# Kernel tuning notes

Hardware: AMD Instinct MI355X
Metric: run time of the kernel (lower is better)

## Reference

```python
import jax, jax.numpy as jnp
import numpy as np

N = 8192       # batch_size
D = 128        # embedding dim
C = 1000       # num classes
EPS = 1e-8     # torch CosineSimilarity eps


def setup_inputs() -> dict:
    key = jax.random.key(0)
    k1, k2, k3, k4 = jax.random.split(key, 4)
    inst_embed = jax.random.normal(k1, (N, D), dtype=jnp.float32)
    proxy = jax.random.normal(k2, (N, D), dtype=jnp.float32)
    # binary mask marking same-class (non-negative) pairs, stored as float
    negative_mask = (jax.random.uniform(k3, (N, C)) < 0.5).astype(jnp.float32)
    labels = jax.random.randint(k4, (N,), 0, C)
    temperature = jnp.float32(0.07)
    margin = jnp.float32(0.0)
    return {
        'inst_embed': inst_embed,
        'proxy': proxy,
        'negative_mask': negative_mask,
        'labels': labels,
        'temperature': temperature,
        'margin': margin,
    }


def _remove_diag(M):
    # M: [h, h] -> [h, h-1], dropping the diagonal, row-major order (as torch bool-mask view)
    h = M.shape[0]
    j = jnp.arange(h - 1)[None, :]
    i = jnp.arange(h)[:, None]
    cols = j + (j >= i)  # skip column i in row i
    return jnp.take_along_axis(M, cols, axis=1)


def _l2_normalize(x):
    return x / jnp.maximum(jnp.linalg.norm(x, axis=-1, keepdims=True), EPS)


def reference(inst_embed, proxy, negative_mask, labels, temperature, margin):
    negative_mask = negative_mask.T                       # [C, N]
    xn = _l2_normalize(inst_embed)                        # [N, D]
    sim = xn @ xn.T                                       # [N, N] cosine similarity matrix
    instance_zone = jnp.exp((_remove_diag(sim) - margin) / temperature)  # [N, N-1]
    pn = _l2_normalize(proxy)
    inst2proxy_positive = jnp.exp((jnp.sum(xn * pn, axis=-1) - margin) / temperature)  # [N]
    # pos_collected_numerator == True branch
    mask_4_remove_negatives = _remove_diag(negative_mask[labels])        # [N, N-1]
    inst2inst_positives = instance_zone * mask_4_remove_negatives
    numerator = inst2proxy_positive + inst2inst_positives.sum(axis=1)
    denominator = inst2proxy_positive + instance_zone.sum(axis=1)
    criterion = -jnp.log(temperature * (numerator / denominator)).mean()
    return criterion
```

## Files before the change

### kernel.cpp

```cpp
#include <hip/hip_runtime.h>
#include <hip/hip_bf16.h>

typedef unsigned short u16;
typedef unsigned int   u32;
typedef unsigned long long u64;
typedef __attribute__((ext_vector_type(8))) short short8;
typedef __attribute__((ext_vector_type(4))) float float4v;

#define N 8192
#define D 128
#define C 1000
#define TILE 128
#define NW64 (N / 64)
#define JQ 4
#define GRIDY 16
#define JW (JQ * 2)
#define LOG2E 1.44269504088896340736f

__global__ void prep_kernel(const float* __restrict__ nm, u64* __restrict__ packed,
                            const float* __restrict__ x, const float* __restrict__ pr,
                            u16* __restrict__ xnb, float* __restrict__ p_out,
                            float* __restrict__ den, float* __restrict__ num,
                            const float* __restrict__ tp, const float* __restrict__ mp) {
    __shared__ u32 Ls[64 * 65];
    const int bid  = blockIdx.x;
    const int lane = threadIdx.x & 63;
    const int wv   = threadIdx.x >> 6;

    if (bid < 2048) {
        const int jt = bid & 127;
        const int lt = bid >> 7;
        const int j0 = jt * 64;
        const int l  = lt * 64 + lane;
        const bool lv = l < C;

        #pragma unroll
        for (int rr = 0; rr < 16; rr++) {
            const int r = wv * 16 + rr;
            float v = lv ? nm[(size_t)(j0 + r) * C + l] : 0.0f;
            Ls[r * 65 + lane] = (v > 0.5f) ? 1u : 0u;
        }
        __syncthreads();
        #pragma unroll
        for (int cc = 0; cc < 16; cc++) {
            const int c = wv * 16 + cc;
            u64 m = __ballot(Ls[lane * 65 + c] != 0u);
            if (lane == 0 && (lt * 64 + c) < C)
                packed[(size_t)(lt * 64 + c) * NW64 + jt] = m;
        }
    } else {
        const int row = (bid - 2048) * 4 + wv;
        const float2* xr  = (const float2*)(x  + (size_t)row * D);
        const float2* prr = (const float2*)(pr + (size_t)row * D);
        float2 xv = xr[lane];
        float2 pv = prr[lane];

        float sx  = xv.x * xv.x + xv.y * xv.y;
        float sp  = pv.x * pv.x + pv.y * pv.y;
        float sxp = xv.x * pv.x + xv.y * pv.y;
        #pragma unroll
        for (int off = 32; off; off >>= 1) {
            sx  += __shfl_xor(sx,  off);
            sp  += __shfl_xor(sp,  off);
            sxp += __shfl_xor(sxp, off);
        }
        float nx = fmaxf(sqrtf(sx), 1e-8f);
        float np = fmaxf(sqrtf(sp), 1e-8f);
        float inv = 1.0f / nx;

        __hip_bfloat16 b0 = __float2bfloat16(xv.x * inv);
        __hip_bfloat16 b1 = __float2bfloat16(xv.y * inv);
        ((__hip_bfloat162*)xnb)[(size_t)row * 64 + lane] = __halves2bfloat162(b0, b1);

        if (lane == 0) {
            float T = tp[0], M = mp[0];
            p_out[row] = __expf((sxp / (nx * np) - M) / T);
            den[row] = 0.0f;
            num[row] = 0.0f;
        }
    }
}

#define AS1 __attribute__((address_space(1)))
#define AS3 __attribute__((address_space(3)))

static __device__ __forceinline__ void load_lds16(const u16* g, u16* l) {
    __builtin_amdgcn_global_load_lds((const AS1 u32*)(const void*)g,
                                     (AS3 u32*)(void*)l, 16, 0, 0);
}

template <bool RELOAD>
__device__ __forceinline__ void mfma_chunk(float4v (&acc)[2][2], const short8 (&a_f)[4][2],
                                           short8 (&bc)[4][2], const u16* Bnext,
                                           const int (&koff)[4]) {
    #pragma unroll
    for (int a = 0; a < 2; a++)
        #pragma unroll
        for (int b = 0; b < 2; b++)
            acc[a][b] = (float4v){0.f, 0.f, 0.f, 0.f};
    #pragma unroll
    for (int kk = 0; kk < 4; kk++) {
        #pragma unroll
        for (int tm = 0; tm < 2; tm++)
            #pragma unroll
            for (int tn = 0; tn < 2; tn++)
                acc[tm][tn] = __builtin_amdgcn_mfma_f32_16x16x32_bf16(
                    a_f[kk][tm], bc[kk][tn], acc[tm][tn], 0, 0, 0);
        if (RELOAD) {
            #pragma unroll
            for (int tn = 0; tn < 2; tn++)
                bc[kk][tn] = *(const short8*)(Bnext + tn * 2048 + koff[kk]);
        }
    }
}

template <bool DIAG, int CI>
__device__ __forceinline__ void epi_chunk(const float4v (&acc)[2][2], const u64* __restrict__ Ms,
                                          float (&dacc)[2][4], float (&nacc)[2][4],
                                          int wv, int kq, int m0,
                                          int ibase, int jbase, int q,
                                          float kA2, float kB2) {
    #pragma unroll
    for (int tm = 0; tm < 2; tm++) {
        #pragma unroll
        for (int r = 0; r < 4; r++) {
            const int lrow = wv * 32 + tm * 16 + kq * 4 + r;
            const u64 ws = Ms[lrow * JW + q * 2 + (CI >> 1)] >> m0;
            const int gi = ibase + lrow;
            #pragma unroll
            for (int tn = 0; tn < 2; tn++) {
                float e = __builtin_amdgcn_exp2f(fmaf(acc[tm][tn][r], kA2, kB2));
                if (DIAG) {
                    const int gj = jbase + CI * 32 + tn * 16 + m0;
                    if (gi == gj) e = 0.0f;
                }
                dacc[tm][r] += e;
                const u32 bit = (u32)(ws >> (((CI & 1) * 2 + tn) * 16)) & 1u;
                nacc[tm][r] = fmaf((float)bit, e, nacc[tm][r]);
            }
        }
    }
}

__global__ __launch_bounds__(256, 2)
void cc_main(const u16* __restrict__ xnb, const int* __restrict__ labels,
             const u64* __restrict__ packed,
             float* __restrict__ den, float* __restrict__ num,
             const float* __restrict__ tp, const float* __restrict__ mp) {
    __shared__ u16 Bs[TILE * D];
    __shared__ u64 Ms[TILE * JW];

    const int tid  = threadIdx.x;
    const int lane = tid & 63;
    const int wv   = tid >> 6;
    const int m0   = lane & 15;
    const int kq   = lane >> 4;
    const int ibase  = blockIdx.x * TILE;
    const int jsplit = blockIdx.y;
    const int jt0    = jsplit * JQ;

    const float T = tp[0];
    const float M = mp[0];
    const float kA2 = LOG2E / T;
    const float kB2 = -M * LOG2E / T;

    #pragma unroll
    for (int t = 0; t < 4; t++) {
        const int idx = t * 256 + tid;
        const int row = idx >> 3, h = idx & 7;
        const int lab = labels[ibase + row];
        Ms[idx] = packed[(size_t)lab * NW64 + jt0 * 2 + h];
    }

    const u16* Alane = xnb + (size_t)(ibase + wv * 32 + m0) * D + kq * 8;
    short8 a_f[4][2];
    #pragma unroll
    for (int kk = 0; kk < 4; kk++)
        #pragma unroll
        for (int tm = 0; tm < 2; tm++)
            a_f[kk][tm] = *(const short8*)(Alane + tm * (16 * D) + kk * 32);

    const int srow  = wv * 4 + (lane >> 4);
    const int sunit = (lane & 15) ^ (srow & 7);
    const u16* Bsrc = xnb + (size_t)srow * D + sunit * 8;
    u16* BsDst = (u16*)Bs + wv * 512;

    const int swz7 = m0 & 7;
    int koff[4];
    #pragma unroll
    for (int kk = 0; kk < 4; kk++) koff[kk] = ((kq + kk * 4) ^ swz7) * 8;
    const u16* LBrd = (const u16*)Bs + m0 * 128;

    float dacc[2][4] = {};
    float nacc[2][4] = {};
    float4v acc[2][2];
    short8 bc[4][2];

    for (int q = 0; q < JQ; q++) {
        const int jt = jt0 + q;
        const int jbase = jt * TILE;
        const bool diag = (jt == blockIdx.x);

        __syncthreads();
        {
            const u16* sq = Bsrc + (size_t)jbase * D;
            #pragma unroll
            for (int rnd = 0; rnd < 8; rnd++)
                load_lds16(sq + rnd * 16 * D, BsDst + rnd * 2048);
        }
        __syncthreads();

        #pragma unroll
        for (int kk = 0; kk < 4; kk++)
            #pragma unroll
            for (int tn = 0; tn < 2; tn++)
                bc[kk][tn] = *(const short8*)(LBrd + tn * 2048 + koff[kk]);

        mfma_chunk<true>(acc, a_f, bc, LBrd + 1 * 4096, koff);
        if (diag) epi_chunk<true , 0>(acc, Ms, dacc, nacc, wv, kq, m0, ibase, jbase, q, kA2, kB2);
        else      epi_chunk<false, 0>(acc, Ms, dacc, nacc, wv, kq, m0, ibase, jbase, q, kA2, kB2);

        mfma_chunk<true>(acc, a_f, bc, LBrd + 2 * 4096, koff);
        if (diag) epi_chunk<true , 1>(acc, Ms, dacc, nacc, wv, kq, m0, ibase, jbase, q, kA2, kB2);
        else      epi_chunk<false, 1>(acc, Ms, dacc, nacc, wv, kq, m0, ibase, jbase, q, kA2, kB2);

        mfma_chunk<true>(acc, a_f, bc, LBrd + 3 * 4096, koff);
        if (diag) epi_chunk<true , 2>(acc, Ms, dacc, nacc, wv, kq, m0, ibase, jbase, q, kA2, kB2);
        else      epi_chunk<false, 2>(acc, Ms, dacc, nacc, wv, kq, m0, ibase, jbase, q, kA2, kB2);

        mfma_chunk<false>(acc, a_f, bc, LBrd, koff);
        if (diag) epi_chunk<true , 3>(acc, Ms, dacc, nacc, wv, kq, m0, ibase, jbase, q, kA2, kB2);
        else      epi_chunk<false, 3>(acc, Ms, dacc, nacc, wv, kq, m0, ibase, jbase, q, kA2, kB2);
    }

    #pragma unroll
    for (int tm = 0; tm < 2; tm++) {
        #pragma unroll
        for (int r = 0; r < 4; r++) {
            float d = dacc[tm][r], n = nacc[tm][r];
            #pragma unroll
            for (int off = 1; off < 16; off <<= 1) {
                d += __shfl_xor(d, off);
                n += __shfl_xor(n, off);
            }
            if (m0 == 0) {
                const int gi = ibase + wv * 32 + tm * 16 + kq * 4 + r;
                atomicAdd(&den[gi], d);
                atomicAdd(&num[gi], n);
            }
        }
    }
}

__global__ void loss_kernel(const float* __restrict__ p, const float* __restrict__ den,
                            const float* __restrict__ num, float* __restrict__ out,
                            const float* __restrict__ tp) {
    __shared__ float red[16];
    const float T = tp[0];
    float s = 0.0f;
    #pragma unroll
    for (int t = 0; t < N / 1024; t++) {
        const int i = t * 1024 + threadIdx.x;
        float pi = p[i];
        s += -__logf(T * (pi + num[i]) / (pi + den[i]));
    }
    #pragma unroll
    for (int off = 32; off; off >>= 1) s += __shfl_xor(s, off);
    const int lane = threadIdx.x & 63, wv = threadIdx.x >> 6;
    if (lane == 0) red[wv] = s;
    __syncthreads();
    if (wv == 0) {
        float t = (lane < 16) ? red[lane] : 0.0f;
        #pragma unroll
        for (int off = 8; off; off >>= 1) t += __shfl_xor(t, off);
        if (lane == 0) out[0] = t / (float)N;
    }
}

extern "C" void kernel_launch(void* const* d_in, const int* in_sizes, int n_in,
                              void* d_out, int out_size, void* d_ws, size_t ws_size,
                              hipStream_t stream) {
    (void)in_sizes; (void)n_in; (void)out_size; (void)ws_size;
    const float* inst   = (const float*)d_in[0];
    const float* proxy  = (const float*)d_in[1];
    const float* nm     = (const float*)d_in[2];
    const int*   labels = (const int*)d_in[3];
    const float* temp   = (const float*)d_in[4];
    const float* marg   = (const float*)d_in[5];
    float* out = (float*)d_out;

    char* ws = (char*)d_ws;
    u16*   xnb    = (u16*)ws;
    float* p_arr  = (float*)(ws + 2097152);
    u64*   packed = (u64*)(ws + 2129920);
    float* den    = (float*)(ws + 3153920);
    float* num    = (float*)(ws + 3186688);

    prep_kernel<<<4096, 256, 0, stream>>>(nm, packed, inst, proxy, xnb, p_arr,
                                          den, num, temp, marg);
    cc_main<<<dim3(N / TILE, GRIDY), 256, 0, stream>>>(xnb, labels, packed, den, num, temp, marg);
    loss_kernel<<<1, 1024, 0, stream>>>(p_arr, den, num, out, temp);
}
```

Before: 126.5 us.

## Double-buffer B tiles, vectorize mask packing, fuse loss into main kernel

The main GEMM loop now splits each 128-row B tile into two 64-row halves held in separate LDS buffers, so the next half loads while the current half is computed, replacing the load-then-compute pattern. The mask-packing stage reads the negative mask with float4 loads for full column blocks. The separate loss kernel is removed: the last block to finish, found through an atomic counter, computes the final reduction. This saves a launch and hides load latency, but the single finishing block runs the whole 8192-element reduction with only 256 threads.

```diff
diff --git a/kernel.cpp b/kernel.cpp
--- a/kernel.cpp
+++ b/kernel.cpp
@@ -14,6 +14,7 @@
 #define NW64 (N / 64)
 #define JQ 4
 #define GRIDY 16
+#define NBLK ((N / TILE) * GRIDY)
 #define JW (JQ * 2)
 #define LOG2E 1.44269504088896340736f
 
@@ -21,6 +22,7 @@
                             const float* __restrict__ x, const float* __restrict__ pr,
                             u16* __restrict__ xnb, float* __restrict__ p_out,
                             float* __restrict__ den, float* __restrict__ num,
+                            int* __restrict__ ctr,
                             const float* __restrict__ tp, const float* __restrict__ mp) {
     __shared__ u32 Ls[64 * 65];
     const int bid  = blockIdx.x;
@@ -31,14 +33,29 @@
         const int jt = bid & 127;
         const int lt = bid >> 7;
         const int j0 = jt * 64;
-        const int l  = lt * 64 + lane;
-        const bool lv = l < C;
-
-        #pragma unroll
-        for (int rr = 0; rr < 16; rr++) {
-            const int r = wv * 16 + rr;
-            float v = lv ? nm[(size_t)(j0 + r) * C + l] : 0.0f;
-            Ls[r * 65 + lane] = (v > 0.5f) ? 1u : 0u;
+        const int l0 = lt * 64;
+
+        if (lt < 15) {
+            const int tid = threadIdx.x;
+            #pragma unroll
+            for (int it = 0; it < 4; it++) {
+                const int r  = it * 16 + (tid >> 4);
+                const int c0 = (tid & 15) * 4;
+                const float4 v = *(const float4*)(nm + (size_t)(j0 + r) * C + l0 + c0);
+                Ls[r * 65 + c0 + 0] = (v.x > 0.5f) ? 1u : 0u;
+                Ls[r * 65 + c0 + 1] = (v.y > 0.5f) ? 1u : 0u;
+                Ls[r * 65 + c0 + 2] = (v.z > 0.5f) ? 1u : 0u;
+                Ls[r * 65 + c0 + 3] = (v.w > 0.5f) ? 1u : 0u;
+            }
+        } else {
+            const int l  = l0 + lane;
+            const bool lv = l < C;
+            #pragma unroll
+            for (int rr = 0; rr < 16; rr++) {
+                const int r = wv * 16 + rr;
+                float v = lv ? nm[(size_t)(j0 + r) * C + l] : 0.0f;
+                Ls[r * 65 + lane] = (v > 0.5f) ? 1u : 0u;
+            }
         }
         __syncthreads();
         #pragma unroll
@@ -49,6 +66,7 @@
                 packed[(size_t)(lt * 64 + c) * NW64 + jt] = m;
         }
     } else {
+        if (bid == 2048 && threadIdx.x == 0) ctr[0] = 0;
         const int row = (bid - 2048) * 4 + wv;
         const float2* xr  = (const float2*)(x  + (size_t)row * D);
         const float2* prr = (const float2*)(pr + (size_t)row * D);
@@ -142,12 +160,33 @@
     }
 }
 
+template <bool DIAG, int H>
+__device__ __forceinline__ void phase_compute(float4v (&acc)[2][2], const short8 (&a_f)[4][2],
+                                              short8 (&bc)[4][2], const u16* LBh,
+                                              const int (&koff)[4], const u64* __restrict__ Ms,
+                                              float (&dacc)[2][4], float (&nacc)[2][4],
+                                              int wv, int kq, int m0,
+                                              int ibase, int jbase, int q,
+                                              float kA2, float kB2) {
+    #pragma unroll
+    for (int kk = 0; kk < 4; kk++)
+        #pragma unroll
+        for (int tn = 0; tn < 2; tn++)
+            bc[kk][tn] = *(const short8*)(LBh + tn * 2048 + koff[kk]);
+    mfma_chunk<true>(acc, a_f, bc, LBh + 4096, koff);
+    epi_chunk<DIAG, H * 2 + 0>(acc, Ms, dacc, nacc, wv, kq, m0, ibase, jbase, q, kA2, kB2);
+    mfma_chunk<false>(acc, a_f, bc, LBh, koff);
+    epi_chunk<DIAG, H * 2 + 1>(acc, Ms, dacc, nacc, wv, kq, m0, ibase, jbase, q, kA2, kB2);
+}
+
 __global__ __launch_bounds__(256, 2)
 void cc_main(const u16* __restrict__ xnb, const int* __restrict__ labels,
              const u64* __restrict__ packed,
              float* __restrict__ den, float* __restrict__ num,
+             const float* __restrict__ p_arr, float* __restrict__ out,
+             int* __restrict__ ctr,
              const float* __restrict__ tp, const float* __restrict__ mp) {
-    __shared__ u16 Bs[TILE * D];
+    __shared__ u16 Bs[2][64 * D];
     __shared__ u64 Ms[TILE * JW];
 
     const int tid  = threadIdx.x;
@@ -164,6 +203,14 @@
     const float kA2 = LOG2E / T;
     const float kB2 = -M * LOG2E / T;
 
+    const u16* Alane = xnb + (size_t)(ibase + wv * 32 + m0) * D + kq * 8;
+    short8 a_f[4][2];
+    #pragma unroll
+    for (int kk = 0; kk < 4; kk++)
+        #pragma unroll
+        for (int tm = 0; tm < 2; tm++)
+            a_f[kk][tm] = *(const short8*)(Alane + tm * (16 * D) + kk * 32);
+
     #pragma unroll
     for (int t = 0; t < 4; t++) {
         const int idx = t * 256 + tid;
@@ -172,65 +219,56 @@
         Ms[idx] = packed[(size_t)lab * NW64 + jt0 * 2 + h];
     }
 
-    const u16* Alane = xnb + (size_t)(ibase + wv * 32 + m0) * D + kq * 8;
-    short8 a_f[4][2];
-    #pragma unroll
-    for (int kk = 0; kk < 4; kk++)
-        #pragma unroll
-        for (int tm = 0; tm < 2; tm++)
-            a_f[kk][tm] = *(const short8*)(Alane + tm * (16 * D) + kk * 32);
-
     const int srow  = wv * 4 + (lane >> 4);
     const int sunit = (lane & 15) ^ (srow & 7);
     const u16* Bsrc = xnb + (size_t)srow * D + sunit * 8;
-    u16* BsDst = (u16*)Bs + wv * 512;
+    u16* Dst0 = &Bs[0][0] + wv * 512;
+    u16* Dst1 = &Bs[1][0] + wv * 512;
 
     const int swz7 = m0 & 7;
     int koff[4];
     #pragma unroll
     for (int kk = 0; kk < 4; kk++) koff[kk] = ((kq + kk * 4) ^ swz7) * 8;
-    const u16* LBrd = (const u16*)Bs + m0 * 128;
+    const u16* LB0 = &Bs[0][0] + m0 * 128;
+    const u16* LB1 = &Bs[1][0] + m0 * 128;
 
     float dacc[2][4] = {};
     float nacc[2][4] = {};
     float4v acc[2][2];
     short8 bc[4][2];
 
+    {
+        const u16* sq = Bsrc + (size_t)(jt0 * TILE) * D;
+        #pragma unroll
+        for (int rnd = 0; rnd < 4; rnd++)
+            load_lds16(sq + rnd * 16 * D, Dst0 + rnd * 2048);
+    }
+    __syncthreads();
+
     for (int q = 0; q < JQ; q++) {
         const int jt = jt0 + q;
         const int jbase = jt * TILE;
         const bool diag = (jt == blockIdx.x);
 
+        {
+            const u16* sq = Bsrc + (size_t)(jbase + 64) * D;
+            #pragma unroll
+            for (int rnd = 0; rnd < 4; rnd++)
+                load_lds16(sq + rnd * 16 * D, Dst1 + rnd * 2048);
+        }
+        if (diag) phase_compute<true , 0>(acc, a_f, bc, LB0, koff, Ms, dacc, nacc, wv, kq, m0, ibase, jbase, q, kA2, kB2);
+        else      phase_compute<false, 0>(acc, a_f, bc, LB0, koff, Ms, dacc, nacc, wv, kq, m0, ibase, jbase, q, kA2, kB2);
         __syncthreads();
-        {
-            const u16* sq = Bsrc + (size_t)jbase * D;
-            #pragma unroll
-            for (int rnd = 0; rnd < 8; rnd++)
-                load_lds16(sq + rnd * 16 * D, BsDst + rnd * 2048);
-        }
+
+        if (q + 1 < JQ) {
+            const u16* sq = Bsrc + (size_t)((jbase + TILE) * D);
+            #pragma unroll
+            for (int rnd = 0; rnd < 4; rnd++)
+                load_lds16(sq + rnd * 16 * D, Dst0 + rnd * 2048);
+        }
+        if (diag) phase_compute<true , 1>(acc, a_f, bc, LB1, koff, Ms, dacc, nacc, wv, kq, m0, ibase, jbase, q, kA2, kB2);
+        else      phase_compute<false, 1>(acc, a_f, bc, LB1, koff, Ms, dacc, nacc, wv, kq, m0, ibase, jbase, q, kA2, kB2);
         __syncthreads();
-
-        #pragma unroll
-        for (int kk = 0; kk < 4; kk++)
-            #pragma unroll
-            for (int tn = 0; tn < 2; tn++)
-                bc[kk][tn] = *(const short8*)(LBrd + tn * 2048 + koff[kk]);
-
-        mfma_chunk<true>(acc, a_f, bc, LBrd + 1 * 4096, koff);
-        if (diag) epi_chunk<true , 0>(acc, Ms, dacc, nacc, wv, kq, m0, ibase, jbase, q, kA2, kB2);
-        else      epi_chunk<false, 0>(acc, Ms, dacc, nacc, wv, kq, m0, ibase, jbase, q, kA2, kB2);
-
-        mfma_chunk<true>(acc, a_f, bc, LBrd + 2 * 4096, koff);
-        if (diag) epi_chunk<true , 1>(acc, Ms, dacc, nacc, wv, kq, m0, ibase, jbase, q, kA2, kB2);
-        else      epi_chunk<false, 1>(acc, Ms, dacc, nacc, wv, kq, m0, ibase, jbase, q, kA2, kB2);
-
-        mfma_chunk<true>(acc, a_f, bc, LBrd + 3 * 4096, koff);
-        if (diag) epi_chunk<true , 2>(acc, Ms, dacc, nacc, wv, kq, m0, ibase, jbase, q, kA2, kB2);
-        else      epi_chunk<false, 2>(acc, Ms, dacc, nacc, wv, kq, m0, ibase, jbase, q, kA2, kB2);
-
-        mfma_chunk<false>(acc, a_f, bc, LBrd, koff);
-        if (diag) epi_chunk<true , 3>(acc, Ms, dacc, nacc, wv, kq, m0, ibase, jbase, q, kA2, kB2);
-        else      epi_chunk<false, 3>(acc, Ms, dacc, nacc, wv, kq, m0, ibase, jbase, q, kA2, kB2);
     }
 
     #pragma unroll
@@ -250,30 +288,30 @@
             }
         }
     }
-}
-
-__global__ void loss_kernel(const float* __restrict__ p, const float* __restrict__ den,
-                            const float* __restrict__ num, float* __restrict__ out,
-                            const float* __restrict__ tp) {
-    __shared__ float red[16];
-    const float T = tp[0];
-    float s = 0.0f;
-    #pragma unroll
-    for (int t = 0; t < N / 1024; t++) {
-        const int i = t * 1024 + threadIdx.x;
-        float pi = p[i];
-        s += -__logf(T * (pi + num[i]) / (pi + den[i]));
-    }
-    #pragma unroll
-    for (int off = 32; off; off >>= 1) s += __shfl_xor(s, off);
-    const int lane = threadIdx.x & 63, wv = threadIdx.x >> 6;
-    if (lane == 0) red[wv] = s;
+
+    __threadfence();
     __syncthreads();
-    if (wv == 0) {
-        float t = (lane < 16) ? red[lane] : 0.0f;
-        #pragma unroll
-        for (int off = 8; off; off >>= 1) t += __shfl_xor(t, off);
-        if (lane == 0) out[0] = t / (float)N;
+    if (tid == 0) {
+        int old = __hip_atomic_fetch_add(ctr, 1, __ATOMIC_ACQ_REL, __HIP_MEMORY_SCOPE_AGENT);
+        *(int*)&Ms[0] = (old == NBLK - 1) ? 1 : 0;
+    }
+    __syncthreads();
+    if (*(int*)&Ms[0]) {
+        float s = 0.0f;
+        #pragma unroll
+        for (int t = 0; t < N / 256; t++) {
+            const int i = t * 256 + tid;
+            float pi = __hip_atomic_load(p_arr + i, __ATOMIC_RELAXED, __HIP_MEMORY_SCOPE_AGENT);
+            float d  = __hip_atomic_load(den + i,  __ATOMIC_RELAXED, __HIP_MEMORY_SCOPE_AGENT);
+            float n  = __hip_atomic_load(num + i,  __ATOMIC_RELAXED, __HIP_MEMORY_SCOPE_AGENT);
+            s += -__logf(T * (pi + n) / (pi + d));
+        }
+        #pragma unroll
+        for (int off = 32; off; off >>= 1) s += __shfl_xor(s, off);
+        float* red = (float*)&Bs[0][0];
+        if (lane == 0) red[wv] = s;
+        __syncthreads();
+        if (tid == 0) out[0] = (red[0] + red[1] + red[2] + red[3]) / (float)N;
     }
 }
 
@@ -295,9 +333,10 @@
     u64*   packed = (u64*)(ws + 2129920);
     float* den    = (float*)(ws + 3153920);
     float* num    = (float*)(ws + 3186688);
+    int*   ctr    = (int*)(ws + 3219456);
 
     prep_kernel<<<4096, 256, 0, stream>>>(nm, packed, inst, proxy, xnb, p_arr,
-                                          den, num, temp, marg);
-    cc_main<<<dim3(N / TILE, GRIDY), 256, 0, stream>>>(xnb, labels, packed, den, num, temp, marg);
-    loss_kernel<<<1, 1024, 0, stream>>>(p_arr, den, num, out, temp);
-}
+                                          den, num, ctr, temp, marg);
+    cc_main<<<dim3(N / TILE, GRIDY), 256, 0, stream>>>(xnb, labels, packed, den, num,
+                                                       p_arr, out, ctr, temp, marg);
+}
```

Result: slower. 205.7 us (+62.6%).
